# Performance work log

Measured on AMD Instinct MI355X. Metric: run time of the kernel, lower is better.

Reference implementation:

```python
import jax, jax.numpy as jnp
import numpy as np

N_NODES = 50000
N_EDGES = 800000
IN_FEATS = 256
OUT_FEATS = 128


def setup_inputs() -> dict:
    key = jax.random.key(0)
    k1, k2, k3, k4 = jax.random.split(key, 4)
    feat = jax.random.normal(k1, (N_NODES, IN_FEATS), dtype=jnp.float32)
    # xavier uniform init for weight [in, out]
    limit = float(np.sqrt(6.0 / (IN_FEATS + OUT_FEATS)))
    weight = jax.random.uniform(k2, (IN_FEATS, OUT_FEATS), minval=-limit, maxval=limit, dtype=jnp.float32)
    bias = jnp.zeros((OUT_FEATS,), dtype=jnp.float32)
    src = jax.random.randint(k3, (N_EDGES,), 0, N_NODES, dtype=jnp.int32)
    dst = jax.random.randint(k4, (N_EDGES,), 0, N_NODES, dtype=jnp.int32)
    return {"feat": feat, "weight": weight, "bias": bias, "src": src, "dst": dst}


def reference(feat, weight, bias, src, dst):
    N = feat.shape[0]
    in_f, out_f = weight.shape
    # right normalization: 1 / out_degree(src node), clamped to >= 1
    deg = jax.ops.segment_sum(jnp.ones(src.shape[0], dtype=feat.dtype), src, num_segments=N)
    norm = (1.0 / jnp.maximum(deg, 1.0))[:, None]  # [N,1]
    if in_f > out_f:
        # transform first (cheaper messages), then normalize + aggregate
        h = jnp.matmul(feat, weight) * norm          # [N, out]
        rst = jax.ops.segment_sum(h[src], dst, num_segments=N)  # scatter-sum over edges
    else:
        h = feat * norm                               # [N, in]
        rst = jax.ops.segment_sum(h[src], dst, num_segments=N)
        rst = jnp.matmul(rst, weight)
    return rst + bias
```

## Files before the change

### kernel.cpp

```cpp
#include <hip/hip_runtime.h>

#define N_NODES 50000
#define N_EDGES 800000
#define IN_F 256
#define OUT_F 128

#define CHUNKS 128
#define EPC (N_EDGES / CHUNKS)
#define BINW (N_NODES / 4)
#define NWORDS (N_NODES / 4)
#define RGB 196
#define HIST_BLOCKS (2 * CHUNKS)
#define CPW8 (CHUNKS / 8)

#define GEMMF_BLOCKS 196
#define SCAT_BLOCKS 782

typedef __attribute__((ext_vector_type(8))) short short8;
typedef __attribute__((ext_vector_type(4))) float float4_t;

__device__ __forceinline__ short f2bf(float f) {
  unsigned u = __builtin_bit_cast(unsigned, f);
  u = u + 0x7FFFu + ((u >> 16) & 1u);
  return (short)(u >> 16);
}

__device__ __forceinline__ float bflo(unsigned u) {
  return __builtin_bit_cast(float, u << 16);
}
__device__ __forceinline__ float bfhi(unsigned u) {
  return __builtin_bit_cast(float, u & 0xFFFF0000u);
}

__global__ __launch_bounds__(512) void hist_kernel(const int* __restrict__ src,
                                                   const int* __restrict__ dst,
                                                   unsigned char* __restrict__ pdst8,
                                                   unsigned char* __restrict__ psrc8,
                                                   unsigned char* __restrict__ rank8,
                                                   int* __restrict__ cursor) {
  __shared__ unsigned bins[BINW];
  int b = blockIdx.x;
  int tid = threadIdx.x;
  if (b == 0 && tid == 0) *cursor = 0;
  int hs = b >> 7;
  int c = b & 127;
  uint4* b4 = (uint4*)bins;
  for (int j = tid; j < BINW / 4; j += 512) b4[j] = (uint4){0u, 0u, 0u, 0u};
  __syncthreads();
  const int* key = hs ? src : dst;
  int e0 = c * EPC;

  auto process = [&](int v, int eI) {
    unsigned sh = (v & 3) * 8;
    unsigned old = atomicAdd(&bins[v >> 2], 1u << sh);
    if (!hs) rank8[eI] = (unsigned char)((old >> sh) & 0xFFu);
  };

#pragma unroll 2
  for (int tile = 0; tile < 3; ++tile) {
    int i = tile * 2048 + tid;
    int k0 = key[e0 + i];
    int k1 = key[e0 + i + 512];
    int k2 = key[e0 + i + 1024];
    int k3 = key[e0 + i + 1536];
    process(k0, e0 + i);
    process(k1, e0 + i + 512);
    process(k2, e0 + i + 1024);
    process(k3, e0 + i + 1536);
  }
  {
    int i = 6144 + tid;
    if (i < EPC) process(key[e0 + i], e0 + i);
  }
  __syncthreads();
  uint4* p128 = (uint4*)((hs ? psrc8 : pdst8) + (size_t)c * N_NODES);
  const uint4* s128 = (const uint4*)bins;
  for (int j = tid; j < BINW / 4; j += 512) p128[j] = s128[j];
}

__global__ __launch_bounds__(512) void gemmred_kernel(const float* __restrict__ feat,
                                                      const float* __restrict__ W,
                                                      unsigned short* __restrict__ h,
                                                      const unsigned char* __restrict__ pdst8,
                                                      const unsigned char* __restrict__ psrc8,
                                                      unsigned char* __restrict__ delta8,
                                                      int* __restrict__ cnt,
                                                      int* __restrict__ row_start,
                                                      int* __restrict__ cursor,
                                                      float* __restrict__ norm) {
  __shared__ uint4 smem4[4096];
  int b = blockIdx.x;
  int tid = threadIdx.x;

  if (b < GEMMF_BLOCKS) {
    short* wl = (short*)smem4;
#pragma unroll
    for (int i = 0; i < 64; ++i) {
      int idx = i * 512 + tid;
      int k = idx >> 7, n = idx & 127;
      int s = k >> 5, q = (k >> 3) & 3, j = k & 7;
      int tt = n >> 4, m = n & 15;
      wl[((s * 8 + tt) * 64 + q * 16 + m) * 8 + j] = f2bf(W[idx]);
    }
    __syncthreads();

    int w = tid >> 6, l = tid & 63;
    int m = l & 15, q = l >> 4;
    long base = (long)b * 256 + w * 32;

    float4_t acc[2][8];
#pragma unroll
    for (int r = 0; r < 2; ++r)
#pragma unroll
      for (int to = 0; to < 8; ++to) acc[r][to] = (float4_t)(0.0f);

    long row0 = base + m;
    long row1 = base + 16 + m;
    long r0c = row0 < N_NODES - 1 ? row0 : N_NODES - 1;
    long r1c = row1 < N_NODES - 1 ? row1 : N_NODES - 1;
    const float* a0p = feat + (size_t)r0c * IN_F;
    const float* a1p = feat + (size_t)r1c * IN_F;
    const short8* wl8 = (const short8*)smem4;

#pragma unroll
    for (int s = 0; s < 8; ++s) {
      int k0 = s * 32 + q * 8;
      float4_t av0a = *(const float4_t*)(a0p + k0);
      float4_t av0b = *(const float4_t*)(a0p + k0 + 4);
      float4_t av1a = *(const float4_t*)(a1p + k0);
      float4_t av1b = *(const float4_t*)(a1p + k0 + 4);
      short8 fa0, fa1;
#pragma unroll
      for (int i = 0; i < 4; ++i) {
        fa0[i] = f2bf(av0a[i]);
        fa0[i + 4] = f2bf(av0b[i]);
        fa1[i] = f2bf(av1a[i]);
        fa1[i + 4] = f2bf(av1b[i]);
      }
#pragma unroll
      for (int to = 0; to < 8; ++to) {
        short8 fb = wl8[(s * 8 + to) * 64 + l];
        acc[0][to] = __builtin_amdgcn_mfma_f32_16x16x32_bf16(fa0, fb, acc[0][to], 0, 0, 0);
        acc[1][to] = __builtin_amdgcn_mfma_f32_16x16x32_bf16(fa1, fb, acc[1][to], 0, 0, 0);
      }
    }

#pragma unroll
    for (int r = 0; r < 2; ++r) {
#pragma unroll
      for (int i = 0; i < 4; ++i) {
        long row = base + r * 16 + q * 4 + i;
        if (row < N_NODES) {
          size_t ho = (size_t)row * OUT_F;
#pragma unroll
          for (int to = 0; to < 8; ++to) {
            h[ho + to * 16 + m] = (unsigned short)f2bf(acc[r][to][i]);
          }
        }
      }
    }
    return;
  }

  int rb = b - GEMMF_BLOCKS;
  int side = rb >= RGB ? 1 : 0;
  int g = rb - side * RGB;
  int w = tid >> 6, l = tid & 63;
  int wd = g * 64 + l;
  bool ok = wd < NWORDS;
  int wdc = ok ? wd : NWORDS - 1;
  const unsigned* P = (const unsigned*)(side == 0 ? pdst8 : psrc8);
  unsigned(*tot)[64] = (unsigned(*)[64])smem4;

  unsigned vals[CPW8];
  unsigned s = 0;
#pragma unroll
  for (int i = 0; i < CPW8; ++i) {
    vals[i] = P[(size_t)(w * CPW8 + i) * NWORDS + wdc];
    s += vals[i];
  }
  tot[w][l] = s;
  __syncthreads();

  if (side == 0) {
    unsigned base = 0;
#pragma unroll
    for (int w2 = 0; w2 < 8; ++w2)
      if (w2 < w) base += tot[w2][l];
    unsigned run = base;
    unsigned* D = (unsigned*)delta8;
    if (ok) {
#pragma unroll
      for (int i = 0; i < CPW8; ++i) {
        D[(size_t)(w * CPW8 + i) * NWORDS + wd] = run;
        run += vals[i];
      }
    }
    if (w == 0) {
      unsigned ftot = 0;
#pragma unroll
      for (int w2 = 0; w2 < 8; ++w2) ftot += tot[w2][l];
      if (!ok) ftot = 0;
      int c0 = ftot & 255, c1 = (ftot >> 8) & 255, c2 = (ftot >> 16) & 255, c3 = ftot >> 24;
      int T = c0 + c1 + c2 + c3;
      int x = T;
#pragma unroll
      for (int off = 1; off < 64; off <<= 1) {
        int y = __shfl_up(x, off);
        if (l >= off) x += y;
      }
      int waveTotal = __shfl(x, 63);
      int sb = 0;
      if (l == 63) sb = atomicAdd(cursor, waveTotal);
      sb = __shfl(sb, 63);
      int E = sb + x - T;
      if (ok) {
        int4 cv = {c0, c1, c2, c3};
        int4 rv = {E, E + c0, E + c0 + c1, E + c0 + c1 + c2};
        ((int4*)cnt)[wd] = cv;
        ((int4*)row_start)[wd] = rv;
      }
    }
  } else {
    if (w == 0 && ok) {
      unsigned ftot = 0;
#pragma unroll
      for (int w2 = 0; w2 < 8; ++w2) ftot += tot[w2][l];
      float4 nv;
      int d0 = ftot & 255, d1 = (ftot >> 8) & 255, d2 = (ftot >> 16) & 255, d3 = (int)(ftot >> 24);
      nv.x = 1.0f / (float)(d0 > 1 ? d0 : 1);
      nv.y = 1.0f / (float)(d1 > 1 ? d1 : 1);
      nv.z = 1.0f / (float)(d2 > 1 ? d2 : 1);
      nv.w = 1.0f / (float)(d3 > 1 ? d3 : 1);
      ((float4*)norm)[wd] = nv;
    }
  }
}

__global__ __launch_bounds__(256) void scat_kernel(const int* __restrict__ src,
                                                   const int* __restrict__ dst,
                                                   const int* __restrict__ row_start,
                                                   const unsigned char* __restrict__ delta8,
                                                   const unsigned char* __restrict__ rank8,
                                                   int* __restrict__ eidx) {
  int gt = blockIdx.x * 256 + threadIdx.x;
  int e = gt * 4;
  if (e >= N_EDGES) return;
  int4 d4 = *(const int4*)(dst + e);
  int4 s4 = *(const int4*)(src + e);
  unsigned rr = *(const unsigned*)(rank8 + e);
  int dd[4] = {d4.x, d4.y, d4.z, d4.w};
  int ss[4] = {s4.x, s4.y, s4.z, s4.w};
#pragma unroll
  for (int k = 0; k < 4; ++k) {
    int c = (e + k) / EPC;
    int d = dd[k];
    int pos = row_start[d] + (int)delta8[(size_t)c * N_NODES + d] + (int)((rr >> (8 * k)) & 0xFFu);
    eidx[pos] = ss[k];
  }
}

__global__ __launch_bounds__(256) void agg_kernel(const unsigned short* __restrict__ h,
                                                  const int* __restrict__ row_start,
                                                  const int* __restrict__ cnt,
                                                  const int* __restrict__ eidx,
                                                  const float* __restrict__ norm,
                                                  const float* __restrict__ bias,
                                                  float* __restrict__ out) {
  int w = threadIdx.x >> 6, l = threadIdx.x & 63;
  int d = blockIdx.x * 4 + w;
  int rs = row_start[d], re = rs + cnt[d];
  const uint4* __restrict__ hu4 = (const uint4*)h;
  int rowsel = l >> 4;
  int cp = l & 15;
  float a0 = 0.f, a1 = 0.f, a2 = 0.f, a3 = 0.f, a4 = 0.f, a5 = 0.f, a6 = 0.f, a7 = 0.f;

  auto acc8 = [&](uint4 v, float nm) {
    a0 = fmaf(bflo(v.x), nm, a0); a1 = fmaf(bfhi(v.x), nm, a1);
    a2 = fmaf(bflo(v.y), nm, a2); a3 = fmaf(bfhi(v.y), nm, a3);
    a4 = fmaf(bflo(v.z), nm, a4); a5 = fmaf(bfhi(v.z), nm, a5);
    a6 = fmaf(bflo(v.w), nm, a6); a7 = fmaf(bfhi(v.w), nm, a7);
  };

  for (int bse = rs; bse < re; bse += 64) {
    int n = re - bse; if (n > 64) n = 64;
    int e = (l < n) ? eidx[bse + l] : 0;
    int quarter = (n + 3) >> 2;
    int j = 0;
    for (; j + 4 <= quarter; j += 4) {
      int i0 = 4 * j + rowsel;
      int s0 = __shfl(e, i0);
      int s1 = __shfl(e, i0 + 4);
      int s2 = __shfl(e, i0 + 8);
      int s3 = __shfl(e, i0 + 12);
      uint4 v0 = hu4[(size_t)s0 * 16 + cp];
      uint4 v1 = hu4[(size_t)s1 * 16 + cp];
      uint4 v2 = hu4[(size_t)s2 * 16 + cp];
      uint4 v3 = hu4[(size_t)s3 * 16 + cp];
      float nm0 = norm[s0], nm1 = norm[s1], nm2 = norm[s2], nm3 = norm[s3];
      if (i0 >= n) v0 = (uint4){0u, 0u, 0u, 0u};
      if (i0 + 4 >= n) v1 = (uint4){0u, 0u, 0u, 0u};
      if (i0 + 8 >= n) v2 = (uint4){0u, 0u, 0u, 0u};
      if (i0 + 12 >= n) v3 = (uint4){0u, 0u, 0u, 0u};
      acc8(v0, nm0);
      acc8(v1, nm1);
      acc8(v2, nm2);
      acc8(v3, nm3);
    }
    for (; j < quarter; ++j) {
      int i0 = 4 * j + rowsel;
      int s0 = __shfl(e, i0);
      uint4 v0 = hu4[(size_t)s0 * 16 + cp];
      float nm0 = norm[s0];
      if (i0 >= n) v0 = (uint4){0u, 0u, 0u, 0u};
      acc8(v0, nm0);
    }
  }
  a0 += __shfl_xor(a0, 16); a1 += __shfl_xor(a1, 16);
  a2 += __shfl_xor(a2, 16); a3 += __shfl_xor(a3, 16);
  a4 += __shfl_xor(a4, 16); a5 += __shfl_xor(a5, 16);
  a6 += __shfl_xor(a6, 16); a7 += __shfl_xor(a7, 16);
  a0 += __shfl_xor(a0, 32); a1 += __shfl_xor(a1, 32);
  a2 += __shfl_xor(a2, 32); a3 += __shfl_xor(a3, 32);
  a4 += __shfl_xor(a4, 32); a5 += __shfl_xor(a5, 32);
  a6 += __shfl_xor(a6, 32); a7 += __shfl_xor(a7, 32);
  if (rowsel == 0) {
    float4 b0 = ((const float4*)bias)[2 * cp];
    float4 b1 = ((const float4*)bias)[2 * cp + 1];
    float4 o0, o1;
    o0.x = a0 + b0.x; o0.y = a1 + b0.y; o0.z = a2 + b0.z; o0.w = a3 + b0.w;
    o1.x = a4 + b1.x; o1.y = a5 + b1.y; o1.z = a6 + b1.z; o1.w = a7 + b1.w;
    float4* op = (float4*)(out + (size_t)d * OUT_F + 8 * cp);
    op[0] = o0;
    op[1] = o1;
  }
}

extern "C" void kernel_launch(void* const* d_in, const int* in_sizes, int n_in,
                              void* d_out, int out_size, void* d_ws, size_t ws_size,
                              hipStream_t stream) {
  const float* feat = (const float*)d_in[0];
  const float* weight = (const float*)d_in[1];
  const float* bias = (const float*)d_in[2];
  const int* src = (const int*)d_in[3];
  const int* dst = (const int*)d_in[4];
  float* out = (float*)d_out;

  char* ws = (char*)d_ws;
  size_t off = 0;
  auto alloc = [&](size_t bytes) -> void* {
    void* p = ws + off;
    off += (bytes + 511) & ~(size_t)511;
    return p;
  };
  int* cursor = (int*)alloc(4);
  int* cnt = (int*)alloc(N_NODES * 4);
  int* row_start = (int*)alloc(N_NODES * 4);
  float* norm = (float*)alloc(N_NODES * 4);
  int* eidx = (int*)alloc(N_EDGES * 4);
  unsigned short* h = (unsigned short*)alloc((size_t)N_NODES * OUT_F * 2);
  unsigned char* pdst8 = (unsigned char*)alloc((size_t)CHUNKS * N_NODES);
  unsigned char* psrc8 = (unsigned char*)alloc((size_t)CHUNKS * N_NODES);
  unsigned char* delta8 = (unsigned char*)alloc((size_t)CHUNKS * N_NODES);
  unsigned char* rank8 = (unsigned char*)alloc((size_t)N_EDGES);
  (void)off; (void)ws_size; (void)in_sizes; (void)n_in; (void)out_size;

  hipLaunchKernelGGL(hist_kernel, dim3(HIST_BLOCKS), dim3(512), 0, stream,
                     src, dst, pdst8, psrc8, rank8, cursor);
  hipLaunchKernelGGL(gemmred_kernel, dim3(GEMMF_BLOCKS + 2 * RGB), dim3(512), 0, stream,
                     feat, weight, h, pdst8, psrc8, delta8, cnt, row_start, cursor, norm);
  hipLaunchKernelGGL(scat_kernel, dim3(SCAT_BLOCKS), dim3(256), 0, stream,
                     src, dst, row_start, delta8, rank8, eidx);
  hipLaunchKernelGGL(agg_kernel, dim3(N_NODES / 4), dim3(256), 0, stream,
                     h, row_start, cnt, eidx, norm, bias, out);
}
```

Baseline: 166.6 us.

## Stage per-chunk delta row in LDS for scatter, assign half-chunks per block

```diff
diff --git a/kernel.cpp b/kernel.cpp
--- a/kernel.cpp
+++ b/kernel.cpp
@@ -14,7 +14,7 @@
 #define CPW8 (CHUNKS / 8)
 
 #define GEMMF_BLOCKS 196
-#define SCAT_BLOCKS 782
+#define HEPC (EPC / 2)
 
 typedef __attribute__((ext_vector_type(8))) short short8;
 typedef __attribute__((ext_vector_type(4))) float float4_t;
@@ -237,26 +237,43 @@
   }
 }
 
-__global__ __launch_bounds__(256) void scat_kernel(const int* __restrict__ src,
+__global__ __launch_bounds__(512) void scat_kernel(const int* __restrict__ src,
                                                    const int* __restrict__ dst,
                                                    const int* __restrict__ row_start,
                                                    const unsigned char* __restrict__ delta8,
                                                    const unsigned char* __restrict__ rank8,
                                                    int* __restrict__ eidx) {
-  int gt = blockIdx.x * 256 + threadIdx.x;
-  int e = gt * 4;
-  if (e >= N_EDGES) return;
-  int4 d4 = *(const int4*)(dst + e);
-  int4 s4 = *(const int4*)(src + e);
-  unsigned rr = *(const unsigned*)(rank8 + e);
-  int dd[4] = {d4.x, d4.y, d4.z, d4.w};
-  int ss[4] = {s4.x, s4.y, s4.z, s4.w};
-#pragma unroll
-  for (int k = 0; k < 4; ++k) {
-    int c = (e + k) / EPC;
-    int d = dd[k];
-    int pos = row_start[d] + (int)delta8[(size_t)c * N_NODES + d] + (int)((rr >> (8 * k)) & 0xFFu);
-    eidx[pos] = ss[k];
+  __shared__ uint4 dl4[N_NODES / 16];
+  int b = blockIdx.x;
+  int tid = threadIdx.x;
+  int c = b >> 1, hb = b & 1;
+  const uint4* rowp = (const uint4*)(delta8 + (size_t)c * N_NODES);
+  for (int j = tid; j < N_NODES / 16; j += 512) dl4[j] = rowp[j];
+  __syncthreads();
+  const unsigned char* dl = (const unsigned char*)dl4;
+  int e0 = c * EPC + hb * HEPC;
+
+  int dsts[6], rks[6], srcs[6], rss[6];
+#pragma unroll
+  for (int k = 0; k < 6; ++k) {
+    int e = e0 + k * 512 + tid;
+    dsts[k] = dst[e];
+    rks[k] = (int)rank8[e];
+  }
+#pragma unroll
+  for (int k = 0; k < 6; ++k) rss[k] = row_start[dsts[k]];
+#pragma unroll
+  for (int k = 0; k < 6; ++k) srcs[k] = src[e0 + k * 512 + tid];
+#pragma unroll
+  for (int k = 0; k < 6; ++k) {
+    int pos = rss[k] + (int)dl[dsts[k]] + rks[k];
+    eidx[pos] = srcs[k];
+  }
+  if (tid < HEPC - 6 * 512) {
+    int e = e0 + 3072 + tid;
+    int d = dst[e];
+    int pos = row_start[d] + (int)dl[d] + (int)rank8[e];
+    eidx[pos] = src[e];
   }
 }
 
@@ -369,7 +386,7 @@
                      src, dst, pdst8, psrc8, rank8, cursor);
   hipLaunchKernelGGL(gemmred_kernel, dim3(GEMMF_BLOCKS + 2 * RGB), dim3(512), 0, stream,
                      feat, weight, h, pdst8, psrc8, delta8, cnt, row_start, cursor, norm);
-  hipLaunchKernelGGL(scat_kernel, dim3(SCAT_BLOCKS), dim3(256), 0, stream,
+  hipLaunchKernelGGL(scat_kernel, dim3(2 * CHUNKS), dim3(512), 0, stream,
                      src, dst, row_start, delta8, rank8, eidx);
   hipLaunchKernelGGL(agg_kernel, dim3(N_NODES / 4), dim3(256), 0, stream,
                      h, row_start, cnt, eidx, norm, bias, out);
```

New measurement: 161.3 us (median of 2 runs). 1.03x faster.
